# Performance work log

Measured on AMD Instinct MI355X. Metric: run time of the kernel, lower is better.

Reference implementation:

```python
import jax, jax.numpy as jnp
import numpy as np

N_NODES = 100000
N_EDGES = 600000
IN_DIM = 128
OUT_DIM = 64


def setup_inputs() -> dict:
    key = jax.random.key(0)
    k1, k2, k3, k4, k5 = jax.random.split(key, 5)
    x = jax.random.normal(k1, (N_NODES, IN_DIM), dtype=jnp.float32)
    edge_index = jax.random.randint(k2, (2, N_EDGES), 0, N_NODES, dtype=jnp.int64)
    edge_weight = jax.random.uniform(k3, (N_EDGES,), dtype=jnp.float32)
    W1 = jax.random.normal(k4, (IN_DIM, IN_DIM), dtype=jnp.float32) / np.sqrt(IN_DIM)
    b1 = jnp.zeros((IN_DIM,), dtype=jnp.float32)
    W2 = jax.random.normal(k5, (IN_DIM, OUT_DIM), dtype=jnp.float32) / np.sqrt(IN_DIM)
    b2 = jnp.zeros((OUT_DIM,), dtype=jnp.float32)
    return {"x": x, "edge_index": edge_index, "edge_weight": edge_weight,
            "W1": W1, "b1": b1, "W2": W2, "b2": b2}


def _spmm(edge_index, edge_weight, h):
    # out[dst] = sum_{e: dst(e)=dst} w_e * h[src(e)]  -- normalized adjacency SpMM
    src, dst = edge_index[0], edge_index[1]
    msg = h[src] * edge_weight[:, None]          # [E, D] gather + scale
    return jax.ops.segment_sum(msg, dst, num_segments=h.shape[0])  # [N, D]


def reference(x, edge_index, edge_weight, W1, b1, W2, b2):
    # Layer 1: GCNConv(in,in) -> ReLU (dropout is identity in eval mode)
    h = _spmm(edge_index, edge_weight, x @ W1) + b1
    h = jax.nn.relu(h)
    # Layer 2: GCNConv(in,out)
    out = _spmm(edge_index, edge_weight, h @ W2) + b2
    return out
```

## Files before the change

### kernel.cpp

```cpp
#include <hip/hip_runtime.h>

#define NN 100000
#define NE 600000
#define DIN 128
#define DOUT 64
#define SCAN_B 512
#define NBLK ((NN + SCAN_B - 1) / SCAN_B)
#define HIST_B ((NE + 255) / 256)
#define G1_BM 128
#define G1B ((NN + G1_BM - 1) / G1_BM)
#define ZB ((NN + 255) / 256)
#define W1B (DIN * DIN / 256)
#define W2B (DIN * DOUT / 256)
#define XS_PITCH 136

typedef __attribute__((ext_vector_type(8))) short bf16x8;
typedef __attribute__((ext_vector_type(4))) short s16x4;
typedef __attribute__((ext_vector_type(4))) float f32x4;
typedef __attribute__((ext_vector_type(2))) float f32x2;

__device__ inline short f2bf(float f) {
  union { float f; unsigned u; } v; v.f = f;
  unsigned r = (v.u + 0x7FFF + ((v.u >> 16) & 1)) >> 16;
  return (short)r;
}
__device__ inline float bf2f(unsigned short u) {
  union { unsigned u; float f; } v; v.u = ((unsigned)u) << 16;
  return v.f;
}
__device__ inline unsigned char f2fp8(float f) {
  unsigned pk = __builtin_amdgcn_cvt_pk_fp8_f32(f, f, 0, false);
  return (unsigned char)(pk & 0xff);
}
__device__ inline bf16x8 pack8(float4 u0, float4 u1) {
  bf16x8 r;
  r[0] = f2bf(u0.x); r[1] = f2bf(u0.y); r[2] = f2bf(u0.z); r[3] = f2bf(u0.w);
  r[4] = f2bf(u1.x); r[5] = f2bf(u1.y); r[6] = f2bf(u1.z); r[7] = f2bf(u1.w);
  return r;
}
__device__ inline void fma_fp8x16(uint4 q, float w, float* acc) {
  f32x2 f;
  f = __builtin_amdgcn_cvt_pk_f32_fp8(q.x, false); acc[0] += w * f[0];  acc[1] += w * f[1];
  f = __builtin_amdgcn_cvt_pk_f32_fp8(q.x, true);  acc[2] += w * f[0];  acc[3] += w * f[1];
  f = __builtin_amdgcn_cvt_pk_f32_fp8(q.y, false); acc[4] += w * f[0];  acc[5] += w * f[1];
  f = __builtin_amdgcn_cvt_pk_f32_fp8(q.y, true);  acc[6] += w * f[0];  acc[7] += w * f[1];
  f = __builtin_amdgcn_cvt_pk_f32_fp8(q.z, false); acc[8] += w * f[0];  acc[9] += w * f[1];
  f = __builtin_amdgcn_cvt_pk_f32_fp8(q.z, true);  acc[10] += w * f[0]; acc[11] += w * f[1];
  f = __builtin_amdgcn_cvt_pk_f32_fp8(q.w, false); acc[12] += w * f[0]; acc[13] += w * f[1];
  f = __builtin_amdgcn_cvt_pk_f32_fp8(q.w, true);  acc[14] += w * f[0]; acc[15] += w * f[1];
}

__global__ __launch_bounds__(256) void prep_kernel(int* __restrict__ cnt,
                                                   const float* __restrict__ W1,
                                                   short* __restrict__ w1t,
                                                   const float* __restrict__ W2,
                                                   short* __restrict__ w2t) {
  const int b = blockIdx.x, t = threadIdx.x;
  if (b < ZB) {
    int i = b * 256 + t;
    if (i < NN) cnt[i] = 0;
  } else if (b < ZB + W1B) {
    int i = (b - ZB) * 256 + t;
    int n = i >> 7, k = i & 127;
    w1t[i] = f2bf(W1[k * DIN + n]);
  } else {
    int i = (b - ZB - W1B) * 256 + t;
    int n = i >> 7, k = i & 127;
    w2t[i] = f2bf(W2[k * DOUT + n]);
  }
}

__global__ __launch_bounds__(256) void hist_gemm1_kernel(const int* __restrict__ ei,
                                                         int* __restrict__ cnt,
                                                         int* __restrict__ rank,
                                                         const float* __restrict__ x,
                                                         const short* __restrict__ w1t,
                                                         unsigned char* __restrict__ h0) {
  const int b = blockIdx.x, t = threadIdx.x;
  if (b >= G1B) {
    int e = (b - G1B) * 256 + t;
    if (e < NE) rank[e] = atomicAdd(&cnt[ei[NE + e]], 1);
    return;
  }
  const int row0 = b * G1_BM;
  const int wave = t >> 6, lane = t & 63;
  const int nlane = lane & 15, quad = lane >> 4;
  const int mbase = wave * 32;
  f32x4 acc[2][8];
#pragma unroll
  for (int mt = 0; mt < 2; ++mt)
#pragma unroll
    for (int nt = 0; nt < 8; ++nt) acc[mt][nt] = (f32x4){0.f, 0.f, 0.f, 0.f};

  const int ra0 = row0 + mbase + nlane;
  const int ra1 = ra0 + 16;
#pragma unroll
  for (int ks = 0; ks < 4; ++ks) {
    const int koff = ks * 32 + quad * 8;
    bf16x8 a0 = (bf16x8){0, 0, 0, 0, 0, 0, 0, 0};
    bf16x8 a1 = (bf16x8){0, 0, 0, 0, 0, 0, 0, 0};
    if (ra0 < NN) {
      float4 u0 = *(const float4*)&x[(size_t)ra0 * DIN + koff];
      float4 u1 = *(const float4*)&x[(size_t)ra0 * DIN + koff + 4];
      a0 = pack8(u0, u1);
    }
    if (ra1 < NN) {
      float4 u0 = *(const float4*)&x[(size_t)ra1 * DIN + koff];
      float4 u1 = *(const float4*)&x[(size_t)ra1 * DIN + koff + 4];
      a1 = pack8(u0, u1);
    }
#pragma unroll
    for (int nt = 0; nt < 8; ++nt) {
      bf16x8 bfr = *(const bf16x8*)&w1t[(size_t)(nt * 16 + nlane) * DIN + koff];
      acc[0][nt] = __builtin_amdgcn_mfma_f32_16x16x32_bf16(a0, bfr, acc[0][nt], 0, 0, 0);
      acc[1][nt] = __builtin_amdgcn_mfma_f32_16x16x32_bf16(a1, bfr, acc[1][nt], 0, 0, 0);
    }
  }
#pragma unroll
  for (int mt = 0; mt < 2; ++mt)
#pragma unroll
    for (int nt = 0; nt < 8; ++nt)
#pragma unroll
      for (int rg = 0; rg < 4; ++rg) {
        int gr = row0 + mbase + mt * 16 + quad * 4 + rg;
        if (gr < NN) h0[(size_t)gr * DIN + nt * 16 + nlane] = f2fp8(acc[mt][nt][rg]);
      }
}

__global__ __launch_bounds__(512) void scan_local_kernel(const int* __restrict__ cnt,
                                                         int* __restrict__ row_ptr,
                                                         int* __restrict__ blk_sum) {
  __shared__ int s[512];
  const int b = blockIdx.x, t = threadIdx.x;
  const int i = b * 512 + t;
  int v = (i < NN) ? cnt[i] : 0;
  s[t] = v;
  __syncthreads();
  for (int off = 1; off < 512; off <<= 1) {
    int u = (t >= off) ? s[t - off] : 0;
    __syncthreads();
    s[t] += u;
    __syncthreads();
  }
  if (i < NN) row_ptr[i] = s[t] - v;
  if (t == 511) blk_sum[b] = s[511];
}

__global__ __launch_bounds__(512) void scan_add_kernel(int* __restrict__ row_ptr,
                                                       const int* __restrict__ blk_sum) {
  __shared__ int s[512];
  const int b = blockIdx.x, t = threadIdx.x;
  s[t] = (t < NBLK) ? blk_sum[t] : 0;
  __syncthreads();
  for (int off = 1; off < 512; off <<= 1) {
    int u = (t >= off) ? s[t - off] : 0;
    __syncthreads();
    s[t] += u;
    __syncthreads();
  }
  int off = (b > 0) ? s[b - 1] : 0;
  const int i = b * 512 + t;
  if (i < NN) row_ptr[i] += off;
  if (b == 0 && t == 0) row_ptr[NN] = NE;
}

__global__ __launch_bounds__(256) void scatter_kernel(const int* __restrict__ ei,
                                                      const float* __restrict__ ew,
                                                      const int* __restrict__ row_ptr,
                                                      const int* __restrict__ rank,
                                                      int2* __restrict__ ep) {
  int e = blockIdx.x * 256 + threadIdx.x;
  if (e >= NE) return;
  int src = ei[e];
  int dst = ei[NE + e];
  int pos = row_ptr[dst] + rank[e];
  ep[pos] = make_int2(src, __float_as_int(ew[e]));
}

__global__ __launch_bounds__(512) void spmm1_gemm2_kernel(const int* __restrict__ rp,
                                                          const int2* __restrict__ ep,
                                                          const unsigned char* __restrict__ h,
                                                          const float* __restrict__ b1,
                                                          const short* __restrict__ w2t,
                                                          short* __restrict__ h2) {
  __shared__ short xs[G1_BM][XS_PITCH];
  const int t = threadIdx.x;
  const int row0 = blockIdx.x * G1_BM;
  const int sub = t >> 3, lane8 = t & 7;
  float bb[16];
  *(float4*)&bb[0]  = *(const float4*)&b1[lane8 * 16];
  *(float4*)&bb[4]  = *(const float4*)&b1[lane8 * 16 + 4];
  *(float4*)&bb[8]  = *(const float4*)&b1[lane8 * 16 + 8];
  *(float4*)&bb[12] = *(const float4*)&b1[lane8 * 16 + 12];

#pragma unroll
  for (int batch = 0; batch < 2; ++batch) {
    const int r = batch * 64 + sub;
    const int row = row0 + r;
    float acc[16];
#pragma unroll
    for (int j = 0; j < 16; ++j) acc[j] = 0.f;
    if (row < NN) {
      const int b0 = rp[row], e1 = rp[row + 1];
      int i = b0;
      for (; i + 4 <= e1; i += 4) {
        int2 p0 = ep[i], p1 = ep[i + 1], p2 = ep[i + 2], p3 = ep[i + 3];
        uint4 q0 = *(const uint4*)&h[(size_t)p0.x * DIN + lane8 * 16];
        uint4 q1 = *(const uint4*)&h[(size_t)p1.x * DIN + lane8 * 16];
        uint4 q2 = *(const uint4*)&h[(size_t)p2.x * DIN + lane8 * 16];
        uint4 q3 = *(const uint4*)&h[(size_t)p3.x * DIN + lane8 * 16];
        fma_fp8x16(q0, __int_as_float(p0.y), acc);
        fma_fp8x16(q1, __int_as_float(p1.y), acc);
        fma_fp8x16(q2, __int_as_float(p2.y), acc);
        fma_fp8x16(q3, __int_as_float(p3.y), acc);
      }
      if (i + 2 <= e1) {
        int2 p0 = ep[i], p1 = ep[i + 1];
        uint4 q0 = *(const uint4*)&h[(size_t)p0.x * DIN + lane8 * 16];
        uint4 q1 = *(const uint4*)&h[(size_t)p1.x * DIN + lane8 * 16];
        fma_fp8x16(q0, __int_as_float(p0.y), acc);
        fma_fp8x16(q1, __int_as_float(p1.y), acc);
        i += 2;
      }
      if (i < e1) {
        int2 p0 = ep[i];
        uint4 q0 = *(const uint4*)&h[(size_t)p0.x * DIN + lane8 * 16];
        fma_fp8x16(q0, __int_as_float(p0.y), acc);
      }
    }
    bf16x8 o0, o1;
#pragma unroll
    for (int j = 0; j < 8; ++j) {
      o0[j] = f2bf(fmaxf(acc[j] + bb[j], 0.f));
      o1[j] = f2bf(fmaxf(acc[8 + j] + bb[8 + j], 0.f));
    }
    *(bf16x8*)&xs[r][lane8 * 16] = o0;
    *(bf16x8*)&xs[r][lane8 * 16 + 8] = o1;
  }
  __syncthreads();

  const int wave = t >> 6, lane = t & 63;
  const int nlane = lane & 15, quad = lane >> 4;
  const int mbase = wave * 16;
  f32x4 acc2[4];
#pragma unroll
  for (int nt = 0; nt < 4; ++nt) acc2[nt] = (f32x4){0.f, 0.f, 0.f, 0.f};
#pragma unroll
  for (int ks = 0; ks < 4; ++ks) {
    const int koff = ks * 32 + quad * 8;
    bf16x8 a0 = *(const bf16x8*)&xs[mbase + nlane][koff];
#pragma unroll
    for (int nt = 0; nt < 4; ++nt) {
      bf16x8 bfr = *(const bf16x8*)&w2t[(size_t)(nt * 16 + nlane) * DIN + koff];
      acc2[nt] = __builtin_amdgcn_mfma_f32_16x16x32_bf16(a0, bfr, acc2[nt], 0, 0, 0);
    }
  }
#pragma unroll
  for (int nt = 0; nt < 4; ++nt)
#pragma unroll
    for (int rg = 0; rg < 4; ++rg) {
      int gr = row0 + mbase + quad * 4 + rg;
      if (gr < NN) h2[(size_t)gr * DOUT + nt * 16 + nlane] = f2bf(acc2[nt][rg]);
    }
}

__global__ __launch_bounds__(256) void spmm2_kernel(const int* __restrict__ rp,
                                                    const int2* __restrict__ ep,
                                                    const short* __restrict__ h,
                                                    const float* __restrict__ bias,
                                                    float* __restrict__ out) {
  const int row = blockIdx.x * 32 + (threadIdx.x >> 3);
  const int lane = threadIdx.x & 7;
  if (row >= NN) return;
  const int b = rp[row], e = rp[row + 1];
  float acc[8];
#pragma unroll
  for (int j = 0; j < 8; ++j) acc[j] = 0.f;
  int i = b;
  for (; i + 4 <= e; i += 4) {
    int2 p0 = ep[i], p1 = ep[i + 1], p2 = ep[i + 2], p3 = ep[i + 3];
    bf16x8 v0 = *(const bf16x8*)&h[(size_t)p0.x * DOUT + lane * 8];
    bf16x8 v1 = *(const bf16x8*)&h[(size_t)p1.x * DOUT + lane * 8];
    bf16x8 v2 = *(const bf16x8*)&h[(size_t)p2.x * DOUT + lane * 8];
    bf16x8 v3 = *(const bf16x8*)&h[(size_t)p3.x * DOUT + lane * 8];
    float w0 = __int_as_float(p0.y), w1 = __int_as_float(p1.y);
    float w2 = __int_as_float(p2.y), w3 = __int_as_float(p3.y);
#pragma unroll
    for (int j = 0; j < 8; ++j)
      acc[j] += w0 * bf2f((unsigned short)v0[j]) + w1 * bf2f((unsigned short)v1[j]) +
                w2 * bf2f((unsigned short)v2[j]) + w3 * bf2f((unsigned short)v3[j]);
  }
  if (i + 2 <= e) {
    int2 p0 = ep[i], p1 = ep[i + 1];
    bf16x8 v0 = *(const bf16x8*)&h[(size_t)p0.x * DOUT + lane * 8];
    bf16x8 v1 = *(const bf16x8*)&h[(size_t)p1.x * DOUT + lane * 8];
    float w0 = __int_as_float(p0.y), w1 = __int_as_float(p1.y);
#pragma unroll
    for (int j = 0; j < 8; ++j)
      acc[j] += w0 * bf2f((unsigned short)v0[j]) + w1 * bf2f((unsigned short)v1[j]);
    i += 2;
  }
  if (i < e) {
    int2 p0 = ep[i];
    bf16x8 v0 = *(const bf16x8*)&h[(size_t)p0.x * DOUT + lane * 8];
    float w0 = __int_as_float(p0.y);
#pragma unroll
    for (int j = 0; j < 8; ++j) acc[j] += w0 * bf2f((unsigned short)v0[j]);
  }
#pragma unroll
  for (int j = 0; j < 8; ++j) acc[j] += bias[lane * 8 + j];
  *(float4*)&out[(size_t)row * DOUT + lane * 8] = make_float4(acc[0], acc[1], acc[2], acc[3]);
  *(float4*)&out[(size_t)row * DOUT + lane * 8 + 4] = make_float4(acc[4], acc[5], acc[6], acc[7]);
}

extern "C" void kernel_launch(void* const* d_in, const int* in_sizes, int n_in,
                              void* d_out, int out_size, void* d_ws, size_t ws_size,
                              hipStream_t stream) {
  const float* x  = (const float*)d_in[0];
  const int*   ei = (const int*)d_in[1];
  const float* ew = (const float*)d_in[2];
  const float* W1 = (const float*)d_in[3];
  const float* b1 = (const float*)d_in[4];
  const float* W2 = (const float*)d_in[5];
  const float* b2 = (const float*)d_in[6];
  float* out = (float*)d_out;

  char* p = (char*)d_ws;
  int*   cnt     = (int*)p;                 p += sizeof(int) * NN;
  int*   row_ptr = (int*)p;                 p += sizeof(int) * (NN + 4);
  int*   blk_sum = (int*)p;                 p += sizeof(int) * (NBLK + 4);
  int*   rank    = (int*)p;                 p += sizeof(int) * NE;
  int2*  ep      = (int2*)p;                p += sizeof(int2) * NE;
  short* w1t     = (short*)p;               p += sizeof(short) * DIN * DIN;
  short* w2t     = (short*)p;               p += sizeof(short) * DIN * DOUT;
  unsigned char* h0 = (unsigned char*)p;    p += (size_t)NN * DIN;
  short* h2      = (short*)p;

  prep_kernel<<<ZB + W1B + W2B, 256, 0, stream>>>(cnt, W1, w1t, W2, w2t);
  hist_gemm1_kernel<<<G1B + HIST_B, 256, 0, stream>>>(ei, cnt, rank, x, w1t, h0);
  scan_local_kernel<<<NBLK, 512, 0, stream>>>(cnt, row_ptr, blk_sum);
  scan_add_kernel<<<NBLK, 512, 0, stream>>>(row_ptr, blk_sum);
  scatter_kernel<<<HIST_B, 256, 0, stream>>>(ei, ew, row_ptr, rank, ep);
  spmm1_gemm2_kernel<<<G1B, 512, 0, stream>>>(row_ptr, ep, h0, b1, w2t, h2);
  spmm2_kernel<<<(NN + 31) / 32, 256, 0, stream>>>(row_ptr, ep, h2, b2, out);
}
```

Baseline: 225.7 us.

## Stage x tile in LDS and overlap histogram atomics with x loads in GEMM1

Restructures the fused GEMM1/histogram kernel so every block issues coalesced float4 loads of a 64-row x tile, then runs a grid-stride slice of the edge histogram atomics while those loads are in flight. It then converts the tile to bf16 in shared memory and feeds the MFMA A operands from LDS. Previously separate blocks handled the histogram, and GEMM blocks did strided per-lane global loads of x. The tile shrinks from 128 to 64 rows, giving more blocks but less reuse of the W1 fragments per block, and adds LDS traffic and a barrier.

```diff
diff --git a/kernel.cpp b/kernel.cpp
--- a/kernel.cpp
+++ b/kernel.cpp
@@ -9,6 +9,7 @@
 #define HIST_B ((NE + 255) / 256)
 #define G1_BM 128
 #define G1B ((NN + G1_BM - 1) / G1_BM)
+#define G1HB ((NN + 63) / 64)
 #define ZB ((NN + 255) / 256)
 #define W1B (DIN * DIN / 256)
 #define W2B (DIN * DOUT / 256)
@@ -31,12 +32,6 @@
 __device__ inline unsigned char f2fp8(float f) {
   unsigned pk = __builtin_amdgcn_cvt_pk_fp8_f32(f, f, 0, false);
   return (unsigned char)(pk & 0xff);
-}
-__device__ inline bf16x8 pack8(float4 u0, float4 u1) {
-  bf16x8 r;
-  r[0] = f2bf(u0.x); r[1] = f2bf(u0.y); r[2] = f2bf(u0.z); r[3] = f2bf(u0.w);
-  r[4] = f2bf(u1.x); r[5] = f2bf(u1.y); r[6] = f2bf(u1.z); r[7] = f2bf(u1.w);
-  return r;
 }
 __device__ inline void fma_fp8x16(uint4 q, float w, float* acc) {
   f32x2 f;
@@ -70,61 +65,63 @@
   }
 }
 
-__global__ __launch_bounds__(256) void hist_gemm1_kernel(const int* __restrict__ ei,
+__global__ __launch_bounds__(256) void gemm1_hist_kernel(const int* __restrict__ ei,
                                                          int* __restrict__ cnt,
                                                          int* __restrict__ rank,
                                                          const float* __restrict__ x,
                                                          const short* __restrict__ w1t,
                                                          unsigned char* __restrict__ h0) {
-  const int b = blockIdx.x, t = threadIdx.x;
-  if (b >= G1B) {
-    int e = (b - G1B) * 256 + t;
-    if (e < NE) rank[e] = atomicAdd(&cnt[ei[NE + e]], 1);
-    return;
-  }
-  const int row0 = b * G1_BM;
+  __shared__ short xs[64][XS_PITCH];
+  const int t = threadIdx.x;
+  const int row0 = blockIdx.x * 64;
+
+  float4 xv[8];
+#pragma unroll
+  for (int i = 0; i < 8; ++i) {
+    int f = t + i * 256;
+    int r = f >> 5, c4 = f & 31;
+    int gr = row0 + r;
+    xv[i] = (gr < NN) ? *(const float4*)&x[(size_t)gr * DIN + c4 * 4]
+                      : make_float4(0.f, 0.f, 0.f, 0.f);
+  }
+
+  for (int e = blockIdx.x * 256 + t; e < NE; e += G1HB * 256)
+    rank[e] = atomicAdd(&cnt[ei[NE + e]], 1);
+
+#pragma unroll
+  for (int i = 0; i < 8; ++i) {
+    int f = t + i * 256;
+    int r = f >> 5, c4 = f & 31;
+    s16x4 s;
+    s.x = f2bf(xv[i].x); s.y = f2bf(xv[i].y); s.z = f2bf(xv[i].z); s.w = f2bf(xv[i].w);
+    *(s16x4*)&xs[r][c4 * 4] = s;
+  }
+  __syncthreads();
+
   const int wave = t >> 6, lane = t & 63;
   const int nlane = lane & 15, quad = lane >> 4;
-  const int mbase = wave * 32;
-  f32x4 acc[2][8];
-#pragma unroll
-  for (int mt = 0; mt < 2; ++mt)
-#pragma unroll
-    for (int nt = 0; nt < 8; ++nt) acc[mt][nt] = (f32x4){0.f, 0.f, 0.f, 0.f};
-
-  const int ra0 = row0 + mbase + nlane;
-  const int ra1 = ra0 + 16;
+  const int mbase = wave * 16;
+  f32x4 acc[8];
+#pragma unroll
+  for (int nt = 0; nt < 8; ++nt) acc[nt] = (f32x4){0.f, 0.f, 0.f, 0.f};
+
 #pragma unroll
   for (int ks = 0; ks < 4; ++ks) {
     const int koff = ks * 32 + quad * 8;
-    bf16x8 a0 = (bf16x8){0, 0, 0, 0, 0, 0, 0, 0};
-    bf16x8 a1 = (bf16x8){0, 0, 0, 0, 0, 0, 0, 0};
-    if (ra0 < NN) {
-      float4 u0 = *(const float4*)&x[(size_t)ra0 * DIN + koff];
-      float4 u1 = *(const float4*)&x[(size_t)ra0 * DIN + koff + 4];
-      a0 = pack8(u0, u1);
-    }
-    if (ra1 < NN) {
-      float4 u0 = *(const float4*)&x[(size_t)ra1 * DIN + koff];
-      float4 u1 = *(const float4*)&x[(size_t)ra1 * DIN + koff + 4];
-      a1 = pack8(u0, u1);
-    }
+    bf16x8 a = *(const bf16x8*)&xs[mbase + nlane][koff];
 #pragma unroll
     for (int nt = 0; nt < 8; ++nt) {
       bf16x8 bfr = *(const bf16x8*)&w1t[(size_t)(nt * 16 + nlane) * DIN + koff];
-      acc[0][nt] = __builtin_amdgcn_mfma_f32_16x16x32_bf16(a0, bfr, acc[0][nt], 0, 0, 0);
-      acc[1][nt] = __builtin_amdgcn_mfma_f32_16x16x32_bf16(a1, bfr, acc[1][nt], 0, 0, 0);
-    }
-  }
-#pragma unroll
-  for (int mt = 0; mt < 2; ++mt)
-#pragma unroll
-    for (int nt = 0; nt < 8; ++nt)
-#pragma unroll
-      for (int rg = 0; rg < 4; ++rg) {
-        int gr = row0 + mbase + mt * 16 + quad * 4 + rg;
-        if (gr < NN) h0[(size_t)gr * DIN + nt * 16 + nlane] = f2fp8(acc[mt][nt][rg]);
-      }
+      acc[nt] = __builtin_amdgcn_mfma_f32_16x16x32_bf16(a, bfr, acc[nt], 0, 0, 0);
+    }
+  }
+#pragma unroll
+  for (int nt = 0; nt < 8; ++nt)
+#pragma unroll
+    for (int rg = 0; rg < 4; ++rg) {
+      int gr = row0 + mbase + quad * 4 + rg;
+      if (gr < NN) h0[(size_t)gr * DIN + nt * 16 + nlane] = f2fp8(acc[nt][rg]);
+    }
 }
 
 __global__ __launch_bounds__(512) void scan_local_kernel(const int* __restrict__ cnt,
@@ -337,7 +334,7 @@
   short* h2      = (short*)p;
 
   prep_kernel<<<ZB + W1B + W2B, 256, 0, stream>>>(cnt, W1, w1t, W2, w2t);
-  hist_gemm1_kernel<<<G1B + HIST_B, 256, 0, stream>>>(ei, cnt, rank, x, w1t, h0);
+  gemm1_hist_kernel<<<G1HB, 256, 0, stream>>>(ei, cnt, rank, x, w1t, h0);
   scan_local_kernel<<<NBLK, 512, 0, stream>>>(cnt, row_ptr, blk_sum);
   scan_add_kernel<<<NBLK, 512, 0, stream>>>(row_ptr, blk_sum);
   scatter_kernel<<<HIST_B, 256, 0, stream>>>(ei, ew, row_ptr, rank, ep);
```

Result: slower. 234.1 us (+3.7%).
